# Performance work log

Measured on AMD Instinct MI355X. Metric: run time of the kernel, lower is better.

Reference implementation:

```python
import jax, jax.numpy as jnp
import numpy as np

B, S, DIM = 4, 2048, 1024
H, HD = 16, 64
MB = 16
NMB = S // MB
DEG, CP = 3, 8
NB = CP + DEG  # 11 basis functions
NKNOTS = CP + 1 + 2 * DEG  # 15
EPS = 1e-6
BASE_LR = 1.0


def bspline(x, knots, degree=DEG):
    # Cox-de Boor recursion; x: (...,), knots: (G,) uniform -> (..., G-1-degree)
    xk = x[..., None]
    G = knots.shape[0]
    b = ((xk >= knots[:-1]) & (xk < knots[1:])).astype(x.dtype)
    for k in range(1, degree + 1):
        left = (xk - knots[: G - 1 - k]) / (knots[k: G - 1] - knots[: G - 1 - k])
        right = (knots[k + 1: G] - xk) / (knots[k + 1: G] - knots[1: G - k])
        b = left * b[..., :-1] + right * b[..., 1:]
    return b


def ln_fwd(x, gamma, beta, eps=EPS):
    mu = x.mean(-1, keepdims=True)
    var = ((x - mu) ** 2).mean(-1, keepdims=True)
    x_hat = (x - mu) / jnp.sqrt(var + eps)
    return gamma * x_hat + beta


def ln_fused_l2_bwd(x, l2_target, gamma, beta, eps=EPS):
    mu = x.mean(-1, keepdims=True)
    var = ((x - mu) ** 2).mean(-1, keepdims=True)
    std = jnp.sqrt(var + eps)
    x_hat = (x - mu) / std
    grad_x_hat = (gamma * x_hat + beta - l2_target) * gamma
    z = (grad_x_hat - grad_x_hat.mean(-1, keepdims=True)
         - x_hat * (grad_x_hat * x_hat).mean(-1, keepdims=True)) / std
    return z


def apply_rope(t, ang):
    # t: (B,H,S,hd), ang: (S, hd//2) rotation angles
    cos, sin = jnp.cos(ang), jnp.sin(ang)
    t1, t2 = t[..., 0::2], t[..., 1::2]
    r1 = t1 * cos - t2 * sin
    r2 = t1 * sin + t2 * cos
    return jnp.stack([r1, r2], axis=-1).reshape(t.shape)


def setup_inputs() -> dict:
    key = jax.random.key(0)
    ks = jax.random.split(key, 8)
    s = 0.02
    x = jax.random.normal(ks[0], (B, S, DIM), dtype=jnp.float32)
    inv_freq = 1.0 / (10000.0 ** (jnp.arange(0, HD, 2, dtype=jnp.float32) / HD))
    pos_frequencies = jnp.arange(S, dtype=jnp.float32)[:, None] * inv_freq[None, :]
    Wq = jax.random.normal(ks[1], (DIM, DIM), dtype=jnp.float32) * s
    Wk = jax.random.normal(ks[2], (DIM, DIM), dtype=jnp.float32) * s
    Wv = jax.random.normal(ks[3], (DIM, DIM), dtype=jnp.float32) * s
    Wo = jax.random.normal(ks[4], (DIM, DIM), dtype=jnp.float32) * s
    lr_W = jax.random.normal(ks[5], (H, 1, DIM), dtype=jnp.float32) * s
    lr_b = jnp.zeros((H, 1), dtype=jnp.float32)
    g_scale = jnp.zeros((MB,), dtype=jnp.float32)
    ttt_gamma = jnp.ones((H, HD), dtype=jnp.float32)
    ttt_beta = jnp.zeros((H, HD), dtype=jnp.float32)
    post_w = jnp.ones((DIM,), dtype=jnp.float32)
    post_b = jnp.zeros((DIM,), dtype=jnp.float32)
    knots = jnp.linspace(-1.0, 1.0, NKNOTS, dtype=jnp.float32)
    coefficients = jax.random.normal(ks[6], (H, NB, HD), dtype=jnp.float32) * s
    return dict(x=x, pos_frequencies=pos_frequencies, Wq=Wq, Wk=Wk, Wv=Wv, Wo=Wo,
                lr_W=lr_W, lr_b=lr_b, g_scale=g_scale, ttt_gamma=ttt_gamma,
                ttt_beta=ttt_beta, post_w=post_w, post_b=post_b,
                coefficients=coefficients, knots=knots)


def reference(x, pos_frequencies, Wq, Wk, Wv, Wo, lr_W, lr_b, g_scale,
              ttt_gamma, ttt_beta, post_w, post_b, coefficients, knots):
    Bx, Sx = x.shape[:2]
    proj = lambda W: (x @ W.T).reshape(Bx, Sx, H, HD).transpose(0, 2, 1, 3)
    Q = apply_rope(proj(Wq), pos_frequencies)
    K = apply_rope(proj(Wk), pos_frequencies)
    V = apply_rope(proj(Wv), pos_frequencies)

    to_mb = lambda t: t.reshape(Bx, H, NMB, MB, HD).transpose(2, 0, 1, 3, 4)
    Qm, Km, Vm = to_mb(Q), to_mb(K), to_mb(V)  # (n,B,H,m,hd)

    # inner-loop learning rates (get_learning_rate)
    x4 = x.reshape(Bx, NMB, MB, DIM)
    lr = BASE_LR * jax.nn.sigmoid(
        jnp.einsum('bnkd,hd->bhnk', x4, lr_W[:, 0, :]) + lr_b.reshape(1, H, 1, 1)) / HD
    gs = jnp.clip(1.0 / jnp.arange(1, MB + 1, dtype=x.dtype) + g_scale, 0.0, None)
    eta = (lr * gs).transpose(2, 0, 1, 3)  # (n,B,H,m)

    gamma = ttt_gamma[None, :, None, :]
    beta = ttt_beta[None, :, None, :]
    W0 = jnp.broadcast_to(coefficients, (Bx, H, NB, HD))

    def step(W, inp):
        Qi, Ki, Vi, ei = inp  # (B,H,m,hd), eta (B,H,m)
        basK = bspline(Ki, knots)                      # (B,H,m,hd,nb)
        Zk = jax.nn.silu(Ki) + jnp.einsum('bhmdn,bhnd->bhmd', basK, W)
        gz = ln_fused_l2_bwd(Zk, Vi - Ki, gamma, beta)  # (B,H,m,hd)
        tok = jnp.einsum('bhm,bhmd,bhmdn->bhmnd', ei, gz, basK)
        cum = jnp.cumsum(tok, axis=2)                  # causal coeff-grad (B,H,m,nb,hd)
        basQ = bspline(Qi, knots)
        Zq = (jax.nn.silu(Qi)
              + jnp.einsum('bhmdn,bhnd->bhmd', basQ, W)
              - jnp.einsum('bhmdn,bhmnd->bhmd', basQ, cum))
        y = Qi + ln_fwd(Zq, gamma, beta)
        return W - cum[:, :, -1], y

    _, ys = jax.lax.scan(step, W0, (Qm, Km, Vm, eta))  # ys: (n,B,H,m,hd)
    out = ys.transpose(1, 0, 3, 2, 4).reshape(Bx, Sx, DIM)

    mu = out.mean(-1, keepdims=True)
    var = ((out - mu) ** 2).mean(-1, keepdims=True)
    out = (out - mu) / jnp.sqrt(var + EPS) * post_w + post_b
    return out @ Wo.T
```

## Files before the change

kernel.cpp:

```cpp
#include <hip/hip_runtime.h>
#include <stdint.h>


typedef unsigned short ushort_t;
typedef short bf16x8 __attribute__((ext_vector_type(8)));
typedef _Float16 f16x8 __attribute__((ext_vector_type(8)));
typedef float f32x4 __attribute__((ext_vector_type(4)));

__device__ __forceinline__ float bf2f(ushort_t u) {
    union { uint32_t i; float f; } v; v.i = ((uint32_t)u) << 16; return v.f;
}
__device__ __forceinline__ ushort_t f2bf(float f) {
    union { float f; uint32_t i; } v; v.f = f;
    uint32_t r = v.i + 0x7FFFu + ((v.i >> 16) & 1u);
    return (ushort_t)(r >> 16);
}

__device__ __forceinline__ float fast_silu(float x) {
    const float e = __builtin_amdgcn_exp2f(-1.4426950408889634f * x);
    return x * __builtin_amdgcn_rcpf(1.0f + e);
}
__device__ __forceinline__ float fast_rsq(float x) {
    return __builtin_amdgcn_rsqf(x);
}

__device__ __forceinline__ void gl16(const ushort_t* g, ushort_t* l) {
    __builtin_amdgcn_global_load_lds(
        (const __attribute__((address_space(1))) void*)g,
        (__attribute__((address_space(3))) void*)l, 16, 0, 0);
}

template <int CTRL>
__device__ __forceinline__ float dpp_add(float v) {
    int p = __builtin_amdgcn_update_dpp(0, __float_as_int(v), CTRL, 0xF, 0xF, false);
    return v + __int_as_float(p);
}
__device__ __forceinline__ float wave_sum(float v) {
    v = dpp_add<0xB1>(v);
    v = dpp_add<0x4E>(v);
    v = dpp_add<0x141>(v);
    v = dpp_add<0x140>(v);
    v = dpp_add<0x142>(v);
    v = dpp_add<0x143>(v);
    return __int_as_float(__builtin_amdgcn_readlane(__float_as_int(v), 63));
}

__device__ __forceinline__ float rdl63(float v) {
    return __int_as_float(__builtin_amdgcn_readlane(__float_as_int(v), 63));
}

__device__ __forceinline__ void wave_sum6(float& s0, float& s1, float& s2,
                                          float& s3, float& s4, float& s5) {
    asm volatile(
        "s_nop 1\n\t"
        "v_add_f32_dpp %0, %0, %0 quad_perm:[1,0,3,2] row_mask:0xf bank_mask:0xf\n\t"
        "v_add_f32_dpp %1, %1, %1 quad_perm:[1,0,3,2] row_mask:0xf bank_mask:0xf\n\t"
        "v_add_f32_dpp %2, %2, %2 quad_perm:[1,0,3,2] row_mask:0xf bank_mask:0xf\n\t"
        "v_add_f32_dpp %3, %3, %3 quad_perm:[1,0,3,2] row_mask:0xf bank_mask:0xf\n\t"
        "v_add_f32_dpp %4, %4, %4 quad_perm:[1,0,3,2] row_mask:0xf bank_mask:0xf\n\t"
        "v_add_f32_dpp %5, %5, %5 quad_perm:[1,0,3,2] row_mask:0xf bank_mask:0xf\n\t"
        "v_add_f32_dpp %0, %0, %0 quad_perm:[2,3,0,1] row_mask:0xf bank_mask:0xf\n\t"
        "v_add_f32_dpp %1, %1, %1 quad_perm:[2,3,0,1] row_mask:0xf bank_mask:0xf\n\t"
        "v_add_f32_dpp %2, %2, %2 quad_perm:[2,3,0,1] row_mask:0xf bank_mask:0xf\n\t"
        "v_add_f32_dpp %3, %3, %3 quad_perm:[2,3,0,1] row_mask:0xf bank_mask:0xf\n\t"
        "v_add_f32_dpp %4, %4, %4 quad_perm:[2,3,0,1] row_mask:0xf bank_mask:0xf\n\t"
        "v_add_f32_dpp %5, %5, %5 quad_perm:[2,3,0,1] row_mask:0xf bank_mask:0xf\n\t"
        "v_add_f32_dpp %0, %0, %0 row_half_mirror row_mask:0xf bank_mask:0xf\n\t"
        "v_add_f32_dpp %1, %1, %1 row_half_mirror row_mask:0xf bank_mask:0xf\n\t"
        "v_add_f32_dpp %2, %2, %2 row_half_mirror row_mask:0xf bank_mask:0xf\n\t"
        "v_add_f32_dpp %3, %3, %3 row_half_mirror row_mask:0xf bank_mask:0xf\n\t"
        "v_add_f32_dpp %4, %4, %4 row_half_mirror row_mask:0xf bank_mask:0xf\n\t"
        "v_add_f32_dpp %5, %5, %5 row_half_mirror row_mask:0xf bank_mask:0xf\n\t"
        "v_add_f32_dpp %0, %0, %0 row_mirror row_mask:0xf bank_mask:0xf\n\t"
        "v_add_f32_dpp %1, %1, %1 row_mirror row_mask:0xf bank_mask:0xf\n\t"
        "v_add_f32_dpp %2, %2, %2 row_mirror row_mask:0xf bank_mask:0xf\n\t"
        "v_add_f32_dpp %3, %3, %3 row_mirror row_mask:0xf bank_mask:0xf\n\t"
        "v_add_f32_dpp %4, %4, %4 row_mirror row_mask:0xf bank_mask:0xf\n\t"
        "v_add_f32_dpp %5, %5, %5 row_mirror row_mask:0xf bank_mask:0xf\n\t"
        "v_add_f32_dpp %0, %0, %0 row_bcast:15 row_mask:0xf bank_mask:0xf bound_ctrl:0\n\t"
        "v_add_f32_dpp %1, %1, %1 row_bcast:15 row_mask:0xf bank_mask:0xf bound_ctrl:0\n\t"
        "v_add_f32_dpp %2, %2, %2 row_bcast:15 row_mask:0xf bank_mask:0xf bound_ctrl:0\n\t"
        "v_add_f32_dpp %3, %3, %3 row_bcast:15 row_mask:0xf bank_mask:0xf bound_ctrl:0\n\t"
        "v_add_f32_dpp %4, %4, %4 row_bcast:15 row_mask:0xf bank_mask:0xf bound_ctrl:0\n\t"
        "v_add_f32_dpp %5, %5, %5 row_bcast:15 row_mask:0xf bank_mask:0xf bound_ctrl:0\n\t"
        "v_add_f32_dpp %0, %0, %0 row_bcast:31 row_mask:0xf bank_mask:0xf bound_ctrl:0\n\t"
        "v_add_f32_dpp %1, %1, %1 row_bcast:31 row_mask:0xf bank_mask:0xf bound_ctrl:0\n\t"
        "v_add_f32_dpp %2, %2, %2 row_bcast:31 row_mask:0xf bank_mask:0xf bound_ctrl:0\n\t"
        "v_add_f32_dpp %3, %3, %3 row_bcast:31 row_mask:0xf bank_mask:0xf bound_ctrl:0\n\t"
        "v_add_f32_dpp %4, %4, %4 row_bcast:31 row_mask:0xf bank_mask:0xf bound_ctrl:0\n\t"
        "v_add_f32_dpp %5, %5, %5 row_bcast:31 row_mask:0xf bank_mask:0xf bound_ctrl:0"
        : "+v"(s0), "+v"(s1), "+v"(s2), "+v"(s3), "+v"(s4), "+v"(s5));
}

__device__ __forceinline__ void wave_sum2(float& s0, float& s1) {
    asm volatile(
        "s_nop 1\n\t"
        "v_add_f32_dpp %0, %0, %0 quad_perm:[1,0,3,2] row_mask:0xf bank_mask:0xf\n\t"
        "v_add_f32_dpp %1, %1, %1 quad_perm:[1,0,3,2] row_mask:0xf bank_mask:0xf\n\t"
        "s_nop 0\n\t"
        "v_add_f32_dpp %0, %0, %0 quad_perm:[2,3,0,1] row_mask:0xf bank_mask:0xf\n\t"
        "v_add_f32_dpp %1, %1, %1 quad_perm:[2,3,0,1] row_mask:0xf bank_mask:0xf\n\t"
        "s_nop 0\n\t"
        "v_add_f32_dpp %0, %0, %0 row_half_mirror row_mask:0xf bank_mask:0xf\n\t"
        "v_add_f32_dpp %1, %1, %1 row_half_mirror row_mask:0xf bank_mask:0xf\n\t"
        "s_nop 0\n\t"
        "v_add_f32_dpp %0, %0, %0 row_mirror row_mask:0xf bank_mask:0xf\n\t"
        "v_add_f32_dpp %1, %1, %1 row_mirror row_mask:0xf bank_mask:0xf\n\t"
        "s_nop 0\n\t"
        "v_add_f32_dpp %0, %0, %0 row_bcast:15 row_mask:0xf bank_mask:0xf bound_ctrl:0\n\t"
        "v_add_f32_dpp %1, %1, %1 row_bcast:15 row_mask:0xf bank_mask:0xf bound_ctrl:0\n\t"
        "s_nop 0\n\t"
        "v_add_f32_dpp %0, %0, %0 row_bcast:31 row_mask:0xf bank_mask:0xf bound_ctrl:0\n\t"
        "v_add_f32_dpp %1, %1, %1 row_bcast:31 row_mask:0xf bank_mask:0xf bound_ctrl:0"
        : "+v"(s0), "+v"(s1));
}

struct Bas4 { float n[4]; int row; };
__device__ __forceinline__ Bas4 bspline4(float x) {
    const float xp1 = x + 1.0f;
    const float s7 = xp1 * 7.0f;
    const float fi = floorf(s7);
    const bool valid = (fi >= 0.0f) && (fi <= 13.0f);
    const float fic = valid ? fi : 0.0f;
    const float t = s7 - fic;
    const float u = 1.0f - t;
    const float t2 = t * t;
    const float t3 = t2 * t;
    const float u3 = u * u * u;
    const float N0 = u3 * 0.16666666666666666f;
    const float N3 = t3 * 0.16666666666666666f;
    const float N1 = fmaf(0.5f, t3, 0.66666666666666666f - t2);
    const float N2 = 1.0f - N0 - N1 - N3;

    Bas4 r;
    const int i = (int)fic;
    const float nv[4] = {N0, N1, N2, N3};
#pragma unroll
    for (int tt = 0; tt < 4; ++tt) {
        const int j = i + tt - 3;
        const bool ok = valid && ((unsigned)j <= 10u);
        r.n[tt] = ok ? nv[tt] : 0.0f;
    }
    r.row = i;
    return r;
}

__device__ __forceinline__ void split_body(
    const float* __restrict__ in, ushort_t* __restrict__ hi,
    ushort_t* __restrict__ lo, int i, int n4)
{
    if (i >= n4) return;
    const float4 f = reinterpret_cast<const float4*>(in)[i];
    const ushort_t h0 = f2bf(f.x), h1 = f2bf(f.y), h2 = f2bf(f.z), h3 = f2bf(f.w);
    ushort4 hv; hv.x = h0; hv.y = h1; hv.z = h2; hv.w = h3;
    ushort4 lv;
    lv.x = f2bf(f.x - bf2f(h0)); lv.y = f2bf(f.y - bf2f(h1));
    lv.z = f2bf(f.z - bf2f(h2)); lv.w = f2bf(f.w - bf2f(h3));
    reinterpret_cast<ushort4*>(hi)[i] = hv;
    reinterpret_cast<ushort4*>(lo)[i] = lv;
}

__global__ __launch_bounds__(256) void prep_kernel(
    const float* __restrict__ x,
    const float* __restrict__ Wq, const float* __restrict__ Wk,
    const float* __restrict__ Wv,
    const float* __restrict__ lrW, const float* __restrict__ lrb,
    const float* __restrict__ gsc, const float* __restrict__ posf,
    ushort_t* __restrict__ xh, ushort_t* __restrict__ xl,
    ushort_t* __restrict__ Wqh, ushort_t* __restrict__ Wql,
    ushort_t* __restrict__ Wkh, ushort_t* __restrict__ Wkl,
    ushort_t* __restrict__ Wvh, ushort_t* __restrict__ Wvl,
    float* __restrict__ eta, float2* __restrict__ rtab)
{
    const int bid = blockIdx.x;
    const int tid = threadIdx.x;
    if (bid < 8192) {
        split_body(x, xh, xl, bid * 256 + tid, 2097152);
    } else if (bid < 9216) {
        split_body(Wq, Wqh, Wql, (bid - 8192) * 256 + tid, 262144);
    } else if (bid < 10240) {
        split_body(Wk, Wkh, Wkl, (bid - 9216) * 256 + tid, 262144);
    } else if (bid < 11264) {
        split_body(Wv, Wvh, Wvl, (bid - 10240) * 256 + tid, 262144);
    } else if (bid < 13312) {
        const int row = (bid - 11264) * 4 + (tid >> 6);
        const int lane = tid & 63;
        float xv[16];
#pragma unroll
        for (int i = 0; i < 16; ++i) xv[i] = x[(size_t)row * 1024 + lane + i * 64];
        const int b = row >> 11, s = row & 2047, n = s >> 4, m = s & 15;
        const float gs = fmaxf(1.0f / (float)(m + 1) + gsc[m], 0.0f);
        for (int h = 0; h < 16; ++h) {
            float acc = 0.0f;
#pragma unroll
            for (int i = 0; i < 16; ++i) acc += xv[i] * lrW[h * 1024 + lane + i * 64];
            acc = wave_sum(acc);
            if (lane == 0) {
                float sig = 1.0f / (1.0f + expf(-(acc + lrb[h])));
                eta[(((size_t)(b * 16 + h)) * 128 + n) * 16 + m] = (sig / 64.0f) * gs;
            }
        }
    } else {
        const int i = (bid - 13312) * 256 + tid;
        const float ang = posf[i];
        rtab[i] = make_float2(cosf(ang), sinf(ang));
    }
}

__global__ __launch_bounds__(256) void cast16_kernel(
    const float* __restrict__ in, ushort_t* __restrict__ out, int n4)
{
    const int i = blockIdx.x * 256 + threadIdx.x;
    if (i >= n4) return;
    const float4 f = reinterpret_cast<const float4*>(in)[i];
    union { _Float16 h[4]; ushort4 u; } cv;
    cv.h[0] = (_Float16)f.x; cv.h[1] = (_Float16)f.y;
    cv.h[2] = (_Float16)f.z; cv.h[3] = (_Float16)f.w;
    reinterpret_cast<ushort4*>(out)[i] = cv.u;
}

#define GEMM_STAGE(B, KO)                                                      \
    gl16(gA_h + (KO), &Ash[B][wlds]);                                          \
    gl16(gA_l + (KO), &Asl[B][wlds]);                                          \
    gl16(gB_h + (KO), &Bsh[B][wlds]);                                          \
    gl16(gB_l + (KO), &Bsl[B][wlds]);

#define GEMM_COMPUTE(B)                                                        \
    {                                                                          \
        bf16x8 bh[2], bl[2];                                                   \
        _Pragma("unroll")                                                      \
        for (int u = 0; u < 2; ++u) {                                          \
            const int br = (wn * 32 + u * 16 + l15) * 32 + lsw * 8;            \
            bh[u] = *reinterpret_cast<const bf16x8*>(&Bsh[B][br]);             \
            bl[u] = *reinterpret_cast<const bf16x8*>(&Bsl[B][br]);             \
        }                                                                      \
        _Pragma("unroll")                                                      \
        for (int t = 0; t < 4; ++t) {                                          \
            const int ar = (wm * 64 + t * 16 + l15) * 32 + lsw * 8;            \
            const bf16x8 ah = *reinterpret_cast<const bf16x8*>(&Ash[B][ar]);   \
            const bf16x8 al = *reinterpret_cast<const bf16x8*>(&Asl[B][ar]);   \
            _Pragma("unroll")                                                  \
            for (int u = 0; u < 2; ++u) {                                      \
                acc[t][u] = __builtin_amdgcn_mfma_f32_16x16x32_bf16(ah, bh[u], acc[t][u], 0, 0, 0); \
                acc[t][u] = __builtin_amdgcn_mfma_f32_16x16x32_bf16(ah, bl[u], acc[t][u], 0, 0, 0); \
                acc[t][u] = __builtin_amdgcn_mfma_f32_16x16x32_bf16(al, bh[u], acc[t][u], 0, 0, 0); \
            }                                                                  \
        }                                                                      \
    }

#define RAW_BAR()                                                              \
    __builtin_amdgcn_s_barrier();                                              \
    asm volatile("" ::: "memory");

#define GEMM_TILE_BODY(Ah_g, Al_g, Bh_g, Bl_g, rowbase, colb)                  \
    __shared__ __align__(16) ushort_t Ash[2][4096];                            \
    __shared__ __align__(16) ushort_t Asl[2][4096];                            \
    __shared__ __align__(16) ushort_t Bsh[2][4096];                            \
    __shared__ __align__(16) ushort_t Bsl[2][4096];                            \
    const int tid = threadIdx.x;                                               \
    const int wv = tid >> 6, ln = tid & 63;                                    \
    const int l15 = ln & 15, lq = ln >> 4;                                     \
    const int lsw = lq ^ ((l15 >> 1) & 3);          \
    const int wm = wv >> 2, wn = wv & 3;                                       \
    const int srow = tid >> 2;                                     \
    const int skseg = (((tid & 3) ^ ((srow >> 1) & 3)) * 8);  \
    const ushort_t* gA_h = (Ah_g) + (size_t)((rowbase) + srow) * 1024 + skseg; \
    const ushort_t* gA_l = (Al_g) + (size_t)((rowbase) + srow) * 1024 + skseg; \
    const ushort_t* gB_h = (Bh_g) + (size_t)((colb) + srow) * 1024 + skseg;    \
    const ushort_t* gB_l = (Bl_g) + (size_t)((colb) + srow) * 1024 + skseg;    \
    const int wlds = wv * 512;                      \
    f32x4 acc[4][2] = {};                                                      \
    GEMM_STAGE(0, 0)                                                           \
    for (int k0 = 0; k0 < 1024; k0 += 64) {                                    \
                                  \
        GEMM_STAGE(1, k0 + 32)                                                 \
        asm volatile("s_waitcnt vmcnt(4)" ::: "memory");    \
        RAW_BAR()                                                              \
        GEMM_COMPUTE(0)                                                        \
        RAW_BAR()                                                              \
                                  \
        if (k0 + 64 < 1024) {                                                  \
            GEMM_STAGE(0, k0 + 64)                                             \
            asm volatile("s_waitcnt vmcnt(4)" ::: "memory");                   \
        } else {                                                               \
            asm volatile("s_waitcnt vmcnt(0)" ::: "memory");                   \
        }                                                                      \
        RAW_BAR()                                                              \
        GEMM_COMPUTE(1)                                                        \
        RAW_BAR()                                                              \
    }

__global__ __launch_bounds__(512) void qkv_rope_kernel(
    const ushort_t* __restrict__ xh, const ushort_t* __restrict__ xl,
    const ushort_t* __restrict__ Wqh, const ushort_t* __restrict__ Wql,
    const ushort_t* __restrict__ Wkh, const ushort_t* __restrict__ Wkl,
    const ushort_t* __restrict__ Wvh, const ushort_t* __restrict__ Wvl,
    const float2* __restrict__ tab,
    float* __restrict__ Qb, float* __restrict__ Kb, float* __restrict__ Vb)
{
    const int cid = blockIdx.y * 64 + blockIdx.x;
    const int swz = (cid & 7) * 192 + (cid >> 3);
    const int rowbase = (swz & 63) * 128;
    const int colbase = (swz >> 6) * 128;
    const int sel = colbase >> 10;
    const ushort_t* WBh = (sel == 0) ? Wqh : (sel == 1) ? Wkh : Wvh;
    const ushort_t* WBl = (sel == 0) ? Wql : (sel == 1) ? Wkl : Wvl;
    float* dst = (sel == 0) ? Qb : (sel == 1) ? Kb : Vb;
    const int colm = colbase & 1023;

    GEMM_TILE_BODY(xh, xl, WBh, WBl, rowbase, colm)

#pragma unroll
    for (int t = 0; t < 4; ++t)
#pragma unroll
        for (int u = 0; u < 2; ++u) {
            const int col = colm + wn * 32 + u * 16 + l15;
            const int d = col & 63, h = col >> 6;
            const int angidx = d >> 1;
            const int odd = d & 1;
#pragma unroll
            for (int r = 0; r < 4; ++r) {
                const int row = rowbase + wm * 64 + t * 16 + lq * 4 + r;
                const int b = row >> 11, s = row & 2047;
                const float2 cs = tab[s * 32 + angidx];
                const float own = acc[t][u][r];
                const float partner = __shfl_xor(own, 1, 64);
                const float res = odd ? (partner * cs.y + own * cs.x)
                                      : (own * cs.x - partner * cs.y);
                const int n = s >> 4, m = s & 15;
                dst[(((size_t)(b * 16 + h)) * 128 + n) * 1024 + m * 64 + d] = res;
            }
        }
}

__global__ __launch_bounds__(1024) void scan_kernel(
    const float* __restrict__ Qb, const float* __restrict__ Kb,
    const float* __restrict__ Vb, const float* __restrict__ eta,
    const float* __restrict__ tg, const float* __restrict__ tb,
    const float* __restrict__ coeff, float* __restrict__ out_pre)
{
    __shared__ __align__(16) float Wl[17 * 64];
    __shared__ __align__(16) float cum[16 * 17 * 64];
    __shared__ __align__(16) float Ucum[16 * 17 * 64];

    const int tid = threadIdx.x;
    const int m = tid >> 6, d = tid & 63;
    const int b = blockIdx.x >> 4, h = blockIdx.x & 15;

    const float gam = tg[h * 64 + d];
    const float bet = tb[h * 64 + d];
    const float gam2 = gam * gam;
    const float G = wave_sum(gam2);

    for (int i = tid; i < 1088; i += 1024)
        Wl[i] = (i >= 192 && i < 896) ? coeff[h * 704 + (i - 192)] : 0.0f;
    {
        const float4 z = {0.0f, 0.0f, 0.0f, 0.0f};
        float4* c4 = (float4*)cum;
        float4* u4 = (float4*)Ucum;
        for (int i = tid; i < 4352; i += 1024) { c4[i] = z; u4[i] = z; }
    }
    __syncthreads();

    const size_t base = ((size_t)(b * 16 + h)) * 131072;
    const float* Qp = Qb + base;
    const float* Kp = Kb + base;
    const float* Vp = Vb + base;
    const float* ep = eta + ((size_t)(b * 16 + h)) * 2048;

    float kf = Kp[tid], vf = Vp[tid], qf = Qp[tid], ei = ep[m];
    int rprev = 0;
    const int cb = m * 1088 + d;

    for (int n = 0; n < 128; ++n) {
        const int n1 = (n < 127) ? n + 1 : n;
        const float kfN = Kp[n1 * 1024 + tid];
        const float vfN = Vp[n1 * 1024 + tid];
        const float qfN = Qp[n1 * 1024 + tid];
        const float eiN = ep[n1 * 16 + m];

        const Bas4 bk = bspline4(kf);
        float zk = fast_silu(kf);
        {
            const float* w = &Wl[bk.row * 64 + d];
            zk = fmaf(bk.n[0], w[0],   zk);
            zk = fmaf(bk.n[1], w[64],  zk);
            zk = fmaf(bk.n[2], w[128], zk);
            zk = fmaf(bk.n[3], w[192], zk);
        }

        const float E = gam * (bet - (vf - kf));
        float s0 = zk, s1 = zk * zk, s2 = gam2 * zk,
              s3 = gam2 * (zk * zk), s4 = E, s5 = E * zk;
        wave_sum6(s0, s1, s2, s3, s4, s5);
        const float r0 = rdl63(s0);
        const float r1 = rdl63(s1);
        const float r2 = rdl63(s2);
        const float r3 = rdl63(s3);
        const float r4 = rdl63(s4);
        const float r5 = rdl63(s5);

        const float mu = r0 * (1.0f / 64.0f);
        const float var = r1 * (1.0f / 64.0f) - mu * mu;
        const float rstd = fast_rsq(var + 1e-6f);
        const float xhat = (zk - mu) * rstd;
        const float gxh = gam2 * xhat + E;
        const float t1 = rstd * (r2 - mu * G) + r4;
        const float t2 = rstd * rstd * (r3 - 2.0f * mu * r2 + mu * mu * G)
                       + rstd * (r5 - mu * r4);
        const float gz = (gxh - t1 * (1.0f / 64.0f) - xhat * (t2 * (1.0f / 64.0f))) * rstd;

        const float tokf = ei * gz;
        {
            float* cz = &cum[cb + rprev * 64];
            cz[0] = 0.0f; cz[64] = 0.0f; cz[128] = 0.0f; cz[192] = 0.0f;
            float* cw = &cum[cb + bk.row * 64];
            cw[0]   = tokf * bk.n[0];
            cw[64]  = tokf * bk.n[1];
            cw[128] = tokf * bk.n[2];
            cw[192] = tokf * bk.n[3];
            rprev = bk.row;
        }
        __syncthreads();

        if (tid < 176) {
            float4* c4 = (float4*)cum;
            float4* u4 = (float4*)Ucum;
            float4* w4 = (float4*)Wl;
            float4 v[16];
#pragma unroll
            for (int mm = 0; mm < 16; ++mm) v[mm] = c4[mm * 272 + 48 + tid];
            float4 a = w4[48 + tid];
#pragma unroll
            for (int mm = 0; mm < 16; ++mm) {
                a.x -= v[mm].x; a.y -= v[mm].y; a.z -= v[mm].z; a.w -= v[mm].w;
                u4[mm * 272 + 48 + tid] = a;
            }
            w4[48 + tid] = a;
        }
        const Bas4 bq = bspline4(qf);
        float zq = fast_silu(qf);
        __syncthreads();

        {
            const float* u = &Ucum[cb + bq.row * 64];
            zq = fmaf(bq.n[0], u[0],   zq);
            zq = fmaf(bq.n[1], u[64],  zq);
            zq = fmaf(bq.n[2], u[128], zq);
            zq = fmaf(bq.n[3], u[192], zq);
        }

        float q0 = zq, q1 = zq * zq;
        wave_sum2(q0, q1);
        const float u1 = rdl63(q0);
        const float u2 = rdl63(q1);
        const float mu2 = u1 * (1.0f / 64.0f);
        const float var2 = u2 * (1.0f / 64.0f) - mu2 * mu2;
        const float rstd2 = fast_rsq(var2 + 1e-6f);
        const float y = qf + gam * (zq - mu2) * rstd2 + bet;
        out_pre[((size_t)b * 2048 + n * 16 + m) * 1024 + h * 64 + d] = y;

        kf = kfN; vf = vfN; qf = qfN; ei = eiN;
    }
}

__global__ __launch_bounds__(256) void ln_kernel(
    const float* __restrict__ in, const float* __restrict__ pw,
    const float* __restrict__ pb, ushort_t* __restrict__ o16)
{
    const int row = blockIdx.x * 4 + (threadIdx.x >> 6);
    const int lane = threadIdx.x & 63;
    const float* r = in + (size_t)row * 1024;
    float v[16];
    float s1 = 0.0f, s2 = 0.0f;
#pragma unroll
    for (int i = 0; i < 16; ++i) {
        v[i] = r[lane + i * 64];
        s1 += v[i];
        s2 += v[i] * v[i];
    }
    s1 = wave_sum(s1);
    s2 = wave_sum(s2);
    const float mu = s1 * (1.0f / 1024.0f);
    const float var = s2 * (1.0f / 1024.0f) - mu * mu;
    const float rstd = rsqrtf(var + 1e-6f);
#pragma unroll
    for (int i = 0; i < 16; ++i) {
        const int c = lane + i * 64;
        const float o = (v[i] - mu) * rstd * pw[c] + pb[c];
        union { _Float16 h; ushort_t u; } cv;
        cv.h = (_Float16)o;
        o16[(size_t)row * 1024 + c] = cv.u;
    }
}

__global__ __launch_bounds__(512) void out_gemm_kernel(
    const ushort_t* __restrict__ Ag, const ushort_t* __restrict__ Bg,
    float* __restrict__ out)
{
    const int cid = blockIdx.y * 64 + blockIdx.x;
    const int swz = (cid & 7) * 64 + (cid >> 3);
    const int rowbase = (swz & 63) * 128;
    const int colbase = (swz >> 6) * 128;

    __shared__ __align__(16) ushort_t Ash[2][4096];
    __shared__ __align__(16) ushort_t Bsh[2][4096];
    const int tid = threadIdx.x;
    const int wv = tid >> 6, ln = tid & 63;
    const int l15 = ln & 15, lq = ln >> 4;
    const int lsw = lq ^ ((l15 >> 1) & 3);
    const int wm = wv >> 2, wn = wv & 3;
    const int srow = tid >> 2;
    const int skseg = (((tid & 3) ^ ((srow >> 1) & 3)) * 8);
    const ushort_t* gA = Ag + (size_t)(rowbase + srow) * 1024 + skseg;
    const ushort_t* gB = Bg + (size_t)(colbase + srow) * 1024 + skseg;
    const int wlds = wv * 512;
    f32x4 acc[4][2] = {};

#define OG_STAGE(B, KO)                                                        \
    gl16(gA + (KO), &Ash[B][wlds]);                                            \
    gl16(gB + (KO), &Bsh[B][wlds]);

#define OG_COMPUTE(B)                                                          \
    {                                                                          \
        f16x8 bh[2];                                                           \
        _Pragma("unroll")                                                      \
        for (int u = 0; u < 2; ++u) {                                          \
            const int br = (wn * 32 + u * 16 + l15) * 32 + lsw * 8;            \
            bh[u] = *reinterpret_cast<const f16x8*>(&Bsh[B][br]);              \
        }                                                                      \
        _Pragma("unroll")                                                      \
        for (int t = 0; t < 4; ++t) {                                          \
            const int ar = (wm * 64 + t * 16 + l15) * 32 + lsw * 8;            \
            const f16x8 ah = *reinterpret_cast<const f16x8*>(&Ash[B][ar]);     \
            _Pragma("unroll")                                                  \
            for (int u = 0; u < 2; ++u)                                        \
                acc[t][u] = __builtin_amdgcn_mfma_f32_16x16x32_f16(ah, bh[u], acc[t][u], 0, 0, 0); \
        }                                                                      \
    }

    OG_STAGE(0, 0)
    for (int k0 = 0; k0 < 1024; k0 += 64) {
        OG_STAGE(1, k0 + 32)
        asm volatile("s_waitcnt vmcnt(2)" ::: "memory");
        RAW_BAR()
        OG_COMPUTE(0)
        RAW_BAR()
        if (k0 + 64 < 1024) {
            OG_STAGE(0, k0 + 64)
            asm volatile("s_waitcnt vmcnt(2)" ::: "memory");
        } else {
            asm volatile("s_waitcnt vmcnt(0)" ::: "memory");
        }
        RAW_BAR()
        OG_COMPUTE(1)
        RAW_BAR()
    }
#undef OG_STAGE
#undef OG_COMPUTE

#pragma unroll
    for (int t = 0; t < 4; ++t)
#pragma unroll
        for (int u = 0; u < 2; ++u) {
            const int col = colbase + wn * 32 + u * 16 + l15;
#pragma unroll
            for (int r = 0; r < 4; ++r) {
                const int row = rowbase + wm * 64 + t * 16 + lq * 4 + r;
                out[(size_t)row * 1024 + col] = acc[t][u][r];
            }
        }
}

extern "C" void kernel_launch(void* const* d_in, const int* in_sizes, int n_in,
                              void* d_out, int out_size, void* d_ws, size_t ws_size,
                              hipStream_t stream) {
    const float* x    = (const float*)d_in[0];
    const float* posf = (const float*)d_in[1];
    const float* Wq   = (const float*)d_in[2];
    const float* Wk   = (const float*)d_in[3];
    const float* Wv   = (const float*)d_in[4];
    const float* Wo   = (const float*)d_in[5];
    const float* lrW  = (const float*)d_in[6];
    const float* lrb  = (const float*)d_in[7];
    const float* gsc  = (const float*)d_in[8];
    const float* tg   = (const float*)d_in[9];
    const float* tb   = (const float*)d_in[10];
    const float* pw   = (const float*)d_in[11];
    const float* pb   = (const float*)d_in[12];
    const float* coeff= (const float*)d_in[13];

    char* ws = (char*)d_ws;
    float*    Qb   = (float*)(ws);
    float*    Kb   = (float*)(ws + 33554432);
    float*    Vb   = (float*)(ws + 67108864);
    ushort_t* xh   = (ushort_t*)(ws + 100663296);
    ushort_t* xl   = (ushort_t*)(ws + 117440512);
    float*    outp = (float*)(ws + 100663296);
    float*    eta  = (float*)(ws + 134217728);
    ushort_t* Wqh  = (ushort_t*)(ws + 134742016);
    ushort_t* Wql  = (ushort_t*)(ws + 136839168);
    ushort_t* Wkh  = (ushort_t*)(ws + 138936320);
    ushort_t* Wkl  = (ushort_t*)(ws + 141033472);
    ushort_t* Wvh  = (ushort_t*)(ws + 143130624);
    ushort_t* Wvl  = (ushort_t*)(ws + 145227776);
    ushort_t* Wo16 = (ushort_t*)(ws + 147324928);
    ushort_t* ln16 = (ushort_t*)(ws);
    float2*   rtab = (float2*)(ws + 147324928);

    prep_kernel<<<13568, 256, 0, stream>>>(x, Wq, Wk, Wv, lrW, lrb, gsc, posf,
                                           xh, xl, Wqh, Wql, Wkh, Wkl, Wvh, Wvl,
                                           eta, rtab);
    qkv_rope_kernel<<<dim3(64, 24), 512, 0, stream>>>(xh, xl, Wqh, Wql, Wkh, Wkl,
                                                      Wvh, Wvl, rtab, Qb, Kb, Vb);
    cast16_kernel<<<1024, 256, 0, stream>>>(Wo, Wo16, 262144);
    scan_kernel<<<64, 1024, 0, stream>>>(Qb, Kb, Vb, eta, tg, tb, coeff, outp);
    ln_kernel<<<2048, 256, 0, stream>>>(outp, pw, pb, ln16);
    out_gemm_kernel<<<dim3(64, 8), 512, 0, stream>>>(ln16, Wo16, (float*)d_out);
}
```

Measured before the change: 562.4 us.

## Use fp16 split-x with single fp16 weights in QKV GEMM; prefetch scan K terms

The QKV projection switches from a 3-MFMA bf16 hi/lo split on both operands to fp16: x is still split into hi/lo fp16 parts, but the weights become a single fp16 cast. This cuts the MFMA count per step from three to two and drops one LDS buffer and one global load stream. Separately, the scan kernel computes the next chunk's K B-spline basis, silu and E term before the barrier, taking them off the critical path. The fp16 weights lose mantissa precision and range compared with the bf16x3 scheme, which risks accuracy.

```diff
diff --git a/kernel.cpp b/kernel.cpp
--- a/kernel.cpp
+++ b/kernel.cpp
@@ -3,17 +3,11 @@
 
 
 typedef unsigned short ushort_t;
-typedef short bf16x8 __attribute__((ext_vector_type(8)));
 typedef _Float16 f16x8 __attribute__((ext_vector_type(8)));
 typedef float f32x4 __attribute__((ext_vector_type(4)));
 
 __device__ __forceinline__ float bf2f(ushort_t u) {
     union { uint32_t i; float f; } v; v.i = ((uint32_t)u) << 16; return v.f;
-}
-__device__ __forceinline__ ushort_t f2bf(float f) {
-    union { float f; uint32_t i; } v; v.f = f;
-    uint32_t r = v.i + 0x7FFFu + ((v.i >> 16) & 1u);
-    return (ushort_t)(r >> 16);
 }
 
 __device__ __forceinline__ float fast_silu(float x) {
@@ -145,19 +139,30 @@
     return r;
 }
 
-__device__ __forceinline__ void split_body(
+__device__ __forceinline__ void split16_body(
     const float* __restrict__ in, ushort_t* __restrict__ hi,
-    ushort_t* __restrict__ lo, int i, int n4)
-{
-    if (i >= n4) return;
+    ushort_t* __restrict__ lo, int i)
+{
     const float4 f = reinterpret_cast<const float4*>(in)[i];
-    const ushort_t h0 = f2bf(f.x), h1 = f2bf(f.y), h2 = f2bf(f.z), h3 = f2bf(f.w);
-    ushort4 hv; hv.x = h0; hv.y = h1; hv.z = h2; hv.w = h3;
-    ushort4 lv;
-    lv.x = f2bf(f.x - bf2f(h0)); lv.y = f2bf(f.y - bf2f(h1));
-    lv.z = f2bf(f.z - bf2f(h2)); lv.w = f2bf(f.w - bf2f(h3));
-    reinterpret_cast<ushort4*>(hi)[i] = hv;
-    reinterpret_cast<ushort4*>(lo)[i] = lv;
+    union { _Float16 h[4]; ushort4 u; } hv, lv;
+    hv.h[0] = (_Float16)f.x; hv.h[1] = (_Float16)f.y;
+    hv.h[2] = (_Float16)f.z; hv.h[3] = (_Float16)f.w;
+    lv.h[0] = (_Float16)(f.x - (float)hv.h[0]);
+    lv.h[1] = (_Float16)(f.y - (float)hv.h[1]);
+    lv.h[2] = (_Float16)(f.z - (float)hv.h[2]);
+    lv.h[3] = (_Float16)(f.w - (float)hv.h[3]);
+    reinterpret_cast<ushort4*>(hi)[i] = hv.u;
+    reinterpret_cast<ushort4*>(lo)[i] = lv.u;
+}
+
+__device__ __forceinline__ void cast16_body(
+    const float* __restrict__ in, ushort_t* __restrict__ out, int i)
+{
+    const float4 f = reinterpret_cast<const float4*>(in)[i];
+    union { _Float16 h[4]; ushort4 u; } cv;
+    cv.h[0] = (_Float16)f.x; cv.h[1] = (_Float16)f.y;
+    cv.h[2] = (_Float16)f.z; cv.h[3] = (_Float16)f.w;
+    reinterpret_cast<ushort4*>(out)[i] = cv.u;
 }
 
 __global__ __launch_bounds__(256) void prep_kernel(
@@ -167,21 +172,20 @@
     const float* __restrict__ lrW, const float* __restrict__ lrb,
     const float* __restrict__ gsc, const float* __restrict__ posf,
     ushort_t* __restrict__ xh, ushort_t* __restrict__ xl,
-    ushort_t* __restrict__ Wqh, ushort_t* __restrict__ Wql,
-    ushort_t* __restrict__ Wkh, ushort_t* __restrict__ Wkl,
-    ushort_t* __restrict__ Wvh, ushort_t* __restrict__ Wvl,
+    ushort_t* __restrict__ Wq16, ushort_t* __restrict__ Wk16,
+    ushort_t* __restrict__ Wv16,
     float* __restrict__ eta, float2* __restrict__ rtab)
 {
     const int bid = blockIdx.x;
     const int tid = threadIdx.x;
     if (bid < 8192) {
-        split_body(x, xh, xl, bid * 256 + tid, 2097152);
+        split16_body(x, xh, xl, bid * 256 + tid);
     } else if (bid < 9216) {
-        split_body(Wq, Wqh, Wql, (bid - 8192) * 256 + tid, 262144);
+        cast16_body(Wq, Wq16, (bid - 8192) * 256 + tid);
     } else if (bid < 10240) {
-        split_body(Wk, Wkh, Wkl, (bid - 9216) * 256 + tid, 262144);
+        cast16_body(Wk, Wk16, (bid - 9216) * 256 + tid);
     } else if (bid < 11264) {
-        split_body(Wv, Wvh, Wvl, (bid - 10240) * 256 + tid, 262144);
+        cast16_body(Wv, Wv16, (bid - 10240) * 256 + tid);
     } else if (bid < 13312) {
         const int row = (bid - 11264) * 4 + (tid >> 6);
         const int lane = tid & 63;
@@ -212,89 +216,17 @@
 {
     const int i = blockIdx.x * 256 + threadIdx.x;
     if (i >= n4) return;
-    const float4 f = reinterpret_cast<const float4*>(in)[i];
-    union { _Float16 h[4]; ushort4 u; } cv;
-    cv.h[0] = (_Float16)f.x; cv.h[1] = (_Float16)f.y;
-    cv.h[2] = (_Float16)f.z; cv.h[3] = (_Float16)f.w;
-    reinterpret_cast<ushort4*>(out)[i] = cv.u;
-}
-
-#define GEMM_STAGE(B, KO)                                                      \
-    gl16(gA_h + (KO), &Ash[B][wlds]);                                          \
-    gl16(gA_l + (KO), &Asl[B][wlds]);                                          \
-    gl16(gB_h + (KO), &Bsh[B][wlds]);                                          \
-    gl16(gB_l + (KO), &Bsl[B][wlds]);
-
-#define GEMM_COMPUTE(B)                                                        \
-    {                                                                          \
-        bf16x8 bh[2], bl[2];                                                   \
-        _Pragma("unroll")                                                      \
-        for (int u = 0; u < 2; ++u) {                                          \
-            const int br = (wn * 32 + u * 16 + l15) * 32 + lsw * 8;            \
-            bh[u] = *reinterpret_cast<const bf16x8*>(&Bsh[B][br]);             \
-            bl[u] = *reinterpret_cast<const bf16x8*>(&Bsl[B][br]);             \
-        }                                                                      \
-        _Pragma("unroll")                                                      \
-        for (int t = 0; t < 4; ++t) {                                          \
-            const int ar = (wm * 64 + t * 16 + l15) * 32 + lsw * 8;            \
-            const bf16x8 ah = *reinterpret_cast<const bf16x8*>(&Ash[B][ar]);   \
-            const bf16x8 al = *reinterpret_cast<const bf16x8*>(&Asl[B][ar]);   \
-            _Pragma("unroll")                                                  \
-            for (int u = 0; u < 2; ++u) {                                      \
-                acc[t][u] = __builtin_amdgcn_mfma_f32_16x16x32_bf16(ah, bh[u], acc[t][u], 0, 0, 0); \
-                acc[t][u] = __builtin_amdgcn_mfma_f32_16x16x32_bf16(ah, bl[u], acc[t][u], 0, 0, 0); \
-                acc[t][u] = __builtin_amdgcn_mfma_f32_16x16x32_bf16(al, bh[u], acc[t][u], 0, 0, 0); \
-            }                                                                  \
-        }                                                                      \
-    }
+    cast16_body(in, out, i);
+}
 
 #define RAW_BAR()                                                              \
     __builtin_amdgcn_s_barrier();                                              \
     asm volatile("" ::: "memory");
 
-#define GEMM_TILE_BODY(Ah_g, Al_g, Bh_g, Bl_g, rowbase, colb)                  \
-    __shared__ __align__(16) ushort_t Ash[2][4096];                            \
-    __shared__ __align__(16) ushort_t Asl[2][4096];                            \
-    __shared__ __align__(16) ushort_t Bsh[2][4096];                            \
-    __shared__ __align__(16) ushort_t Bsl[2][4096];                            \
-    const int tid = threadIdx.x;                                               \
-    const int wv = tid >> 6, ln = tid & 63;                                    \
-    const int l15 = ln & 15, lq = ln >> 4;                                     \
-    const int lsw = lq ^ ((l15 >> 1) & 3);          \
-    const int wm = wv >> 2, wn = wv & 3;                                       \
-    const int srow = tid >> 2;                                     \
-    const int skseg = (((tid & 3) ^ ((srow >> 1) & 3)) * 8);  \
-    const ushort_t* gA_h = (Ah_g) + (size_t)((rowbase) + srow) * 1024 + skseg; \
-    const ushort_t* gA_l = (Al_g) + (size_t)((rowbase) + srow) * 1024 + skseg; \
-    const ushort_t* gB_h = (Bh_g) + (size_t)((colb) + srow) * 1024 + skseg;    \
-    const ushort_t* gB_l = (Bl_g) + (size_t)((colb) + srow) * 1024 + skseg;    \
-    const int wlds = wv * 512;                      \
-    f32x4 acc[4][2] = {};                                                      \
-    GEMM_STAGE(0, 0)                                                           \
-    for (int k0 = 0; k0 < 1024; k0 += 64) {                                    \
-                                  \
-        GEMM_STAGE(1, k0 + 32)                                                 \
-        asm volatile("s_waitcnt vmcnt(4)" ::: "memory");    \
-        RAW_BAR()                                                              \
-        GEMM_COMPUTE(0)                                                        \
-        RAW_BAR()                                                              \
-                                  \
-        if (k0 + 64 < 1024) {                                                  \
-            GEMM_STAGE(0, k0 + 64)                                             \
-            asm volatile("s_waitcnt vmcnt(4)" ::: "memory");                   \
-        } else {                                                               \
-            asm volatile("s_waitcnt vmcnt(0)" ::: "memory");                   \
-        }                                                                      \
-        RAW_BAR()                                                              \
-        GEMM_COMPUTE(1)                                                        \
-        RAW_BAR()                                                              \
-    }
-
 __global__ __launch_bounds__(512) void qkv_rope_kernel(
     const ushort_t* __restrict__ xh, const ushort_t* __restrict__ xl,
-    const ushort_t* __restrict__ Wqh, const ushort_t* __restrict__ Wql,
-    const ushort_t* __restrict__ Wkh, const ushort_t* __restrict__ Wkl,
-    const ushort_t* __restrict__ Wvh, const ushort_t* __restrict__ Wvl,
+    const ushort_t* __restrict__ Wq16, const ushort_t* __restrict__ Wk16,
+    const ushort_t* __restrict__ Wv16,
     const float2* __restrict__ tab,
     float* __restrict__ Qb, float* __restrict__ Kb, float* __restrict__ Vb)
 {
@@ -303,12 +235,71 @@
     const int rowbase = (swz & 63) * 128;
     const int colbase = (swz >> 6) * 128;
     const int sel = colbase >> 10;
-    const ushort_t* WBh = (sel == 0) ? Wqh : (sel == 1) ? Wkh : Wvh;
-    const ushort_t* WBl = (sel == 0) ? Wql : (sel == 1) ? Wkl : Wvl;
+    const ushort_t* WB = (sel == 0) ? Wq16 : (sel == 1) ? Wk16 : Wv16;
     float* dst = (sel == 0) ? Qb : (sel == 1) ? Kb : Vb;
     const int colm = colbase & 1023;
 
-    GEMM_TILE_BODY(xh, xl, WBh, WBl, rowbase, colm)
+    __shared__ __align__(16) ushort_t Ash[2][4096];
+    __shared__ __align__(16) ushort_t Asl[2][4096];
+    __shared__ __align__(16) ushort_t Bsh[2][4096];
+    const int tid = threadIdx.x;
+    const int wv = tid >> 6, ln = tid & 63;
+    const int l15 = ln & 15, lq = ln >> 4;
+    const int lsw = lq ^ ((l15 >> 1) & 3);
+    const int wm = wv >> 2, wn = wv & 3;
+    const int srow = tid >> 2;
+    const int skseg = (((tid & 3) ^ ((srow >> 1) & 3)) * 8);
+    const ushort_t* gA_h = xh + (size_t)(rowbase + srow) * 1024 + skseg;
+    const ushort_t* gA_l = xl + (size_t)(rowbase + srow) * 1024 + skseg;
+    const ushort_t* gB   = WB + (size_t)(colm + srow) * 1024 + skseg;
+    const int wlds = wv * 512;
+    f32x4 acc[4][2] = {};
+
+#define QK_STAGE(B, KO)                                                        \
+    gl16(gA_h + (KO), &Ash[B][wlds]);                                          \
+    gl16(gA_l + (KO), &Asl[B][wlds]);                                          \
+    gl16(gB + (KO), &Bsh[B][wlds]);
+
+#define QK_COMPUTE(B)                                                          \
+    {                                                                          \
+        f16x8 bh[2];                                                           \
+        _Pragma("unroll")                                                      \
+        for (int u = 0; u < 2; ++u) {                                          \
+            const int br = (wn * 32 + u * 16 + l15) * 32 + lsw * 8;            \
+            bh[u] = *reinterpret_cast<const f16x8*>(&Bsh[B][br]);              \
+        }                                                                      \
+        _Pragma("unroll")                                                      \
+        for (int t = 0; t < 4; ++t) {                                          \
+            const int ar = (wm * 64 + t * 16 + l15) * 32 + lsw * 8;            \
+            const f16x8 ah = *reinterpret_cast<const f16x8*>(&Ash[B][ar]);     \
+            const f16x8 al = *reinterpret_cast<const f16x8*>(&Asl[B][ar]);     \
+            _Pragma("unroll")                                                  \
+            for (int u = 0; u < 2; ++u) {                                      \
+                acc[t][u] = __builtin_amdgcn_mfma_f32_16x16x32_f16(ah, bh[u], acc[t][u], 0, 0, 0); \
+                acc[t][u] = __builtin_amdgcn_mfma_f32_16x16x32_f16(al, bh[u], acc[t][u], 0, 0, 0); \
+            }                                                                  \
+        }                                                                      \
+    }
+
+    QK_STAGE(0, 0)
+    for (int k0 = 0; k0 < 1024; k0 += 64) {
+        QK_STAGE(1, k0 + 32)
+        asm volatile("s_waitcnt vmcnt(3)" ::: "memory");
+        RAW_BAR()
+        QK_COMPUTE(0)
+        RAW_BAR()
+        if (k0 + 64 < 1024) {
+            QK_STAGE(0, k0 + 64)
+            asm volatile("s_waitcnt vmcnt(3)" ::: "memory");
+        } else {
+            asm volatile("s_waitcnt vmcnt(0)" ::: "memory");
+        }
+        RAW_BAR()
+        QK_COMPUTE(1)
+        RAW_BAR()
+    }
+#undef QK_STAGE
+#undef QK_COMPUTE
 
 #pragma unroll
     for (int t = 0; t < 4; ++t)
@@ -372,6 +363,10 @@
     int rprev = 0;
     const int cb = m * 1088 + d;
 
+    Bas4 bk = bspline4(kf);
+    float szk = fast_silu(kf);
+    float E = gam * (bet - (vf - kf));
+
     for (int n = 0; n < 128; ++n) {
         const int n1 = (n < 127) ? n + 1 : n;
         const float kfN = Kp[n1 * 1024 + tid];
@@ -379,8 +374,7 @@
         const float qfN = Qp[n1 * 1024 + tid];
         const float eiN = ep[n1 * 16 + m];
 
-        const Bas4 bk = bspline4(kf);
-        float zk = fast_silu(kf);
+        float zk = szk;
         {
             const float* w = &Wl[bk.row * 64 + d];
             zk = fmaf(bk.n[0], w[0],   zk);
@@ -389,7 +383,6 @@
             zk = fmaf(bk.n[3], w[192], zk);
         }
 
-        const float E = gam * (bet - (vf - kf));
         float s0 = zk, s1 = zk * zk, s2 = gam2 * zk,
               s3 = gam2 * (zk * zk), s4 = E, s5 = E * zk;
         wave_sum6(s0, s1, s2, s3, s4, s5);
@@ -440,6 +433,9 @@
         }
         const Bas4 bq = bspline4(qf);
         float zq = fast_silu(qf);
+        const Bas4 bkN = bspline4(kfN);
+        const float szkN = fast_silu(kfN);
+        const float EN = gam * (bet - (vfN - kfN));
         __syncthreads();
 
         {
@@ -461,6 +457,7 @@
         out_pre[((size_t)b * 2048 + n * 16 + m) * 1024 + h * 64 + d] = y;
 
         kf = kfN; vf = vfN; qf = qfN; ei = eiN;
+        bk = bkN; szk = szkN; E = EN;
     }
 }
 
@@ -598,21 +595,17 @@
     ushort_t* xl   = (ushort_t*)(ws + 117440512);
     float*    outp = (float*)(ws + 100663296);
     float*    eta  = (float*)(ws + 134217728);
-    ushort_t* Wqh  = (ushort_t*)(ws + 134742016);
-    ushort_t* Wql  = (ushort_t*)(ws + 136839168);
-    ushort_t* Wkh  = (ushort_t*)(ws + 138936320);
-    ushort_t* Wkl  = (ushort_t*)(ws + 141033472);
-    ushort_t* Wvh  = (ushort_t*)(ws + 143130624);
-    ushort_t* Wvl  = (ushort_t*)(ws + 145227776);
+    ushort_t* Wq16 = (ushort_t*)(ws + 134742016);
+    ushort_t* Wk16 = (ushort_t*)(ws + 136839168);
+    ushort_t* Wv16 = (ushort_t*)(ws + 138936320);
     ushort_t* Wo16 = (ushort_t*)(ws + 147324928);
     ushort_t* ln16 = (ushort_t*)(ws);
     float2*   rtab = (float2*)(ws + 147324928);
 
     prep_kernel<<<13568, 256, 0, stream>>>(x, Wq, Wk, Wv, lrW, lrb, gsc, posf,
-                                           xh, xl, Wqh, Wql, Wkh, Wkl, Wvh, Wvl,
-                                           eta, rtab);
-    qkv_rope_kernel<<<dim3(64, 24), 512, 0, stream>>>(xh, xl, Wqh, Wql, Wkh, Wkl,
-                                                      Wvh, Wvl, rtab, Qb, Kb, Vb);
+                                           xh, xl, Wq16, Wk16, Wv16, eta, rtab);
+    qkv_rope_kernel<<<dim3(64, 24), 512, 0, stream>>>(xh, xl, Wq16, Wk16, Wv16,
+                                                      rtab, Qb, Kb, Vb);
     cast16_kernel<<<1024, 256, 0, stream>>>(Wo, Wo16, 262144);
     scan_kernel<<<64, 1024, 0, stream>>>(Qb, Kb, Vb, eta, tg, tb, coeff, outp);
     ln_kernel<<<2048, 256, 0, stream>>>(outp, pw, pb, ln16);
```

Result: faster. 543.6 us (-3.3%).
